# Kernel tuning notes

Hardware: AMD Instinct MI355X
Metric: run time of the kernel (lower is better)

## Reference

```python
import jax, jax.numpy as jnp
import numpy as np

B, N, HID, H, DH, NB = 4, 4096, 768, 12, 64, 266
EPS = 1e-4


def softmax_kernel(data, proj, is_query):
    # data: [B,H,N,DH], proj: [NB,DH]. FAVOR+ positive softmax features.
    d = data.shape[-1]
    ratio = proj.shape[0] ** -0.5
    dn = d ** -0.25  # data normalizer
    data_dash = jnp.einsum('bhnd,jd->bhnj', data * dn, proj)  # [B,H,N,NB]
    diag = 0.5 * jnp.sum((data * dn) ** 2, axis=-1, keepdims=True)  # [B,H,N,1]
    if is_query:
        m = jnp.max(data_dash, axis=-1, keepdims=True)
    else:
        m = jnp.max(data_dash, axis=(-1, -2), keepdims=True)
    return ratio * (jnp.exp(data_dash - diag - m) + EPS)


def setup_inputs() -> dict:
    key = jax.random.key(0)
    ks = jax.random.split(key, 8)
    s = HID ** -0.5
    return {
        'hidden_states': jax.random.normal(ks[0], (B, N, HID), jnp.float32),
        'Wq': jax.random.normal(ks[1], (HID, HID), jnp.float32) * s,
        'bq': jnp.zeros((HID,), jnp.float32),
        'Wk': jax.random.normal(ks[2], (HID, HID), jnp.float32) * s,
        'bk': jnp.zeros((HID,), jnp.float32),
        'Wv': jax.random.normal(ks[3], (HID, HID), jnp.float32) * s,
        'bv': jnp.zeros((HID,), jnp.float32),
        'proj': jax.random.normal(ks[4], (NB, DH), jnp.float32),
    }


def reference(hidden_states, Wq, bq, Wk, bk, Wv, bv, proj):
    def heads(x):  # [B,N,HID] -> [B,H,N,DH]
        return x.reshape(B, N, H, DH).transpose(0, 2, 1, 3)

    q = heads(hidden_states @ Wq.T + bq)
    k = heads(hidden_states @ Wk.T + bk)
    v = heads(hidden_states @ Wv.T + bv)

    qp = softmax_kernel(q, proj, True)   # [B,H,N,NB]
    kp = softmax_kernel(k, proj, False)  # [B,H,N,NB]

    # non-causal linear attention: out = q' (k'^T v) / (q' sum_n k')
    k_sum = jnp.sum(kp, axis=2)                               # [B,H,NB]
    d_inv = 1.0 / jnp.einsum('bhnj,bhj->bhn', qp, k_sum)      # [B,H,N]
    ctx = jnp.einsum('bhnj,bhnd->bhjd', kp, v)                # [B,H,NB,DH]
    out = jnp.einsum('bhnj,bhjd->bhnd', qp, ctx) * d_inv[..., None]

    return out.transpose(0, 2, 1, 3).reshape(B, N, HID)
```

## Files before the change

kernel.cpp:

```cpp
#include <hip/hip_runtime.h>
#include <hip/hip_bf16.h>
#include <stdint.h>

#define B_   4
#define N_   4096
#define HID_ 768
#define H_   12
#define DH_  64
#define NB_  266
#define NBP_ 288
#define EPS_ 1e-4f
#define RATIO_ 0.06131393f

typedef unsigned short u16;
typedef __attribute__((ext_vector_type(8))) short short8;
typedef __attribute__((ext_vector_type(4))) float floatx4;

__device__ __forceinline__ u16 f2b(float f) {
  __hip_bfloat16 h = __float2bfloat16(f);
  return *reinterpret_cast<u16*>(&h);
}
__device__ __forceinline__ float b2f(u16 u) {
  union { unsigned u; float f; } x; x.u = ((unsigned)u) << 16; return x.f;
}
__device__ __forceinline__ unsigned fmap(float x) {
  unsigned u = __float_as_uint(x);
  return (u & 0x80000000u) ? ~u : (u | 0x80000000u);
}
__device__ __forceinline__ float funmap(unsigned u) {
  unsigned b = (u & 0x80000000u) ? (u & 0x7FFFFFFFu) : ~u;
  return __uint_as_float(b);
}
__device__ __forceinline__ void gl16(const u16* g, u16* l) {
  __builtin_amdgcn_global_load_lds(
      (const __attribute__((address_space(1))) void*)g,
      (__attribute__((address_space(3))) void*)l, 16, 0, 0);
}

__global__ void k_convert4(const float4* __restrict__ src, uint2* __restrict__ dst, int n4) {
  int i = blockIdx.x * 256 + threadIdx.x;
  if (i >= n4) return;
  float4 v = src[i];
  union { u16 s[4]; uint2 u; } pk;
  pk.s[0] = f2b(v.x); pk.s[1] = f2b(v.y); pk.s[2] = f2b(v.z); pk.s[3] = f2b(v.w);
  dst[i] = pk.u;
}

__global__ void k_prep_proj(const float* __restrict__ proj, u16* __restrict__ dst) {
  int i = blockIdx.x * 256 + threadIdx.x;
  if (i >= NBP_ * DH_) return;
  int j = i / DH_, d = i - j * DH_;
  float v = (j < NB_) ? proj[j * DH_ + d] * 0.35355339059327373f : 0.f;
  dst[i] = f2b(v);
}

__global__ void k_init(float* __restrict__ zf, unsigned* __restrict__ mbuf, int nf) {
  int i = blockIdx.x * 256 + threadIdx.x;
  if (i < nf) zf[i] = 0.f;
  if (i < B_ * H_) mbuf[i] = 0u;
}

__global__ __launch_bounds__(256) void k_qkv(
    const u16* __restrict__ hsb, const u16* __restrict__ wb,
    const float* __restrict__ bq, const float* __restrict__ bk, const float* __restrict__ bv,
    u16* __restrict__ qb, u16* __restrict__ kb, u16* __restrict__ vT) {
  __shared__ u16 At[128 * 32];
  __shared__ u16 Bt[128 * 32];
  const int m0 = blockIdx.x * 128;
  const int bn = blockIdx.y;
  const int sel = bn / 6;
  const int or0 = (bn % 6) * 128;
  const u16* W = wb + (size_t)sel * HID_ * HID_;
  const int t = threadIdx.x, lane = t & 63, wv = t >> 6;
  const int wr = (wv >> 1) * 64, wc = (wv & 1) * 64;
  const int lm = lane & 15, lq = lane >> 4;
  const int srow = wv * 32 + (lane >> 2);
  const int scol = (lane & 3) * 8;
  const u16* gA0 = hsb + (size_t)(m0 + srow) * HID_ + scol;
  const u16* gA1 = gA0 + 16 * HID_;
  const u16* gB0 = W + (size_t)(or0 + srow) * HID_ + scol;
  const u16* gB1 = gB0 + 16 * HID_;
  u16* lA = At + wv * 1024;
  u16* lB = Bt + wv * 1024;
  floatx4 acc[4][4];
#pragma unroll
  for (int i = 0; i < 4; i++)
#pragma unroll
    for (int j = 0; j < 4; j++) acc[i][j] = (floatx4){0.f, 0.f, 0.f, 0.f};

  for (int k0 = 0; k0 < HID_; k0 += 32) {
    __syncthreads();
    gl16(gA0 + k0, lA);
    gl16(gA1 + k0, lA + 512);
    gl16(gB0 + k0, lB);
    gl16(gB1 + k0, lB + 512);
    __syncthreads();
    short8 af[4], bfr[4];
#pragma unroll
    for (int mt = 0; mt < 4; mt++) af[mt] = *(const short8*)&At[(wr + mt * 16 + lm) * 32 + lq * 8];
#pragma unroll
    for (int nt = 0; nt < 4; nt++) bfr[nt] = *(const short8*)&Bt[(wc + nt * 16 + lm) * 32 + lq * 8];
#pragma unroll
    for (int mt = 0; mt < 4; mt++)
#pragma unroll
      for (int nt = 0; nt < 4; nt++)
        acc[mt][nt] = __builtin_amdgcn_mfma_f32_16x16x32_bf16(af[mt], bfr[nt], acc[mt][nt], 0, 0, 0);
  }
  if (sel < 2) {
    const float* bias = (sel == 0) ? bq : bk;
    u16* dst = (sel == 0) ? qb : kb;
#pragma unroll
    for (int mt = 0; mt < 4; mt++) {
#pragma unroll
      for (int nt = 0; nt < 4; nt++) {
        int lc = or0 + wc + nt * 16 + lm;
        float bb = bias[lc];
#pragma unroll
        for (int r = 0; r < 4; r++) {
          int row = m0 + wr + mt * 16 + lq * 4 + r;
          dst[(size_t)row * HID_ + lc] = f2b(acc[mt][nt][r] + bb);
        }
      }
    }
  } else {
#pragma unroll
    for (int mt = 0; mt < 4; mt++) {
#pragma unroll
      for (int nt = 0; nt < 4; nt++) {
        int lc = or0 + wc + nt * 16 + lm;
        int hh = lc >> 6, dv = lc & 63;
        float bb = bv[lc];
        int rowbase = m0 + wr + mt * 16 + lq * 4;
        int b = rowbase >> 12, n = rowbase & 4095;
        union { u16 s[4]; uint2 u; } pk;
#pragma unroll
        for (int r = 0; r < 4; r++) pk.s[r] = f2b(acc[mt][nt][r] + bb);
        *(uint2*)(vT + ((size_t)(b * H_ + hh) * DH_ + dv) * N_ + n) = pk.u;
      }
    }
  }
}

__global__ __launch_bounds__(256) void k_kmax2(
    const u16* __restrict__ kb, const u16* __restrict__ projb, unsigned* __restrict__ mbuf) {
  const int bh = blockIdx.y, b = bh / H_, h = bh - b * H_;
  const int n0 = blockIdx.x * 256;
  const int t = threadIdx.x, lane = t & 63, wv = t >> 6;
  const int lm = lane & 15, lq = lane >> 4;
  const u16* kbase = kb + (size_t)(b * N_ + n0 + wv * 64) * HID_ + h * DH_;
  short8 af0[4], af1[4];
#pragma unroll
  for (int mt = 0; mt < 4; mt++) {
    const u16* p = kbase + (size_t)(mt * 16 + lm) * HID_ + lq * 8;
    af0[mt] = *(const short8*)p;
    af1[mt] = *(const short8*)(p + 32);
  }
  float mx = -3e38f;
  for (int ct = 0; ct < 17; ct++) {
    const u16* pp = projb + (ct * 16 + lm) * DH_ + lq * 8;
    short8 bf0 = *(const short8*)pp;
    short8 bf1 = *(const short8*)(pp + 32);
    bool valid = (ct < 16) || (lm < 10);
#pragma unroll
    for (int mt = 0; mt < 4; mt++) {
      floatx4 a = __builtin_amdgcn_mfma_f32_16x16x32_bf16(af0[mt], bf0, (floatx4){0.f,0.f,0.f,0.f}, 0, 0, 0);
      a = __builtin_amdgcn_mfma_f32_16x16x32_bf16(af1[mt], bf1, a, 0, 0, 0);
      if (valid) {
#pragma unroll
        for (int r = 0; r < 4; r++) mx = fmaxf(mx, a[r]);
      }
    }
  }
#pragma unroll
  for (int o = 1; o < 64; o <<= 1) mx = fmaxf(mx, __shfl_xor(mx, o));
  if (lane == 0) atomicMax(&mbuf[bh], fmap(mx));
}

__global__ __launch_bounds__(256) void k_ctx3(
    const u16* __restrict__ kb, const u16* __restrict__ vT, const u16* __restrict__ projb,
    const unsigned* __restrict__ mbuf, float* __restrict__ ctxTf, float* __restrict__ ksum) {
  __shared__ u16 kpl[NBP_ * 72];
  const int bh = blockIdx.y, b = bh / H_, h = bh - b * H_;
  const int n0 = blockIdx.x * 256;
  const int t = threadIdx.x, lane = t & 63, wv = t >> 6;
  const int lm = lane & 15, lq = lane >> 4;
  const float m = funmap(mbuf[bh]);
  const u16* vTb = vT + ((size_t)bh * DH_ + wv * 16 + lm) * N_;
  floatx4 acc[18];
#pragma unroll
  for (int jt = 0; jt < 18; jt++) acc[jt] = (floatx4){0.f, 0.f, 0.f, 0.f};
  float kacc[17];
#pragma unroll
  for (int ct = 0; ct < 17; ct++) kacc[ct] = 0.f;

  for (int it = 0; it < 4; it++) {
    const int n64 = n0 + it * 64;
    __syncthreads();
    {
      const int row = n64 + wv * 16 + lm;
      const u16* kr = kb + ((size_t)(b * N_) + row) * HID_ + h * DH_ + lq * 8;
      short8 af0 = *(const short8*)kr;
      short8 af1 = *(const short8*)(kr + 32);
      float rs = 0.f;
#pragma unroll
      for (int i = 0; i < 8; i++) { float f = b2f(((const u16*)&af0)[i]); rs += f * f; }
#pragma unroll
      for (int i = 0; i < 8; i++) { float f = b2f(((const u16*)&af1)[i]); rs += f * f; }
      rs += __shfl_xor(rs, 16);
      rs += __shfl_xor(rs, 32);
      float dg[4];
#pragma unroll
      for (int r = 0; r < 4; r++) dg[r] = 0.0625f * __shfl(rs, lq * 4 + r);
#pragma unroll
      for (int ct = 0; ct < 17; ct++) {
        const u16* pp = projb + (ct * 16 + lm) * DH_ + lq * 8;
        short8 bf0 = *(const short8*)pp;
        short8 bf1 = *(const short8*)(pp + 32);
        floatx4 a = __builtin_amdgcn_mfma_f32_16x16x32_bf16(af0, bf0, (floatx4){0.f,0.f,0.f,0.f}, 0, 0, 0);
        a = __builtin_amdgcn_mfma_f32_16x16x32_bf16(af1, bf1, a, 0, 0, 0);
        bool valid = (ct < 16) || (lm < 10);
        union { u16 s[4]; uint2 u; } pk;
        float kss = 0.f;
#pragma unroll
        for (int r = 0; r < 4; r++) {
          float val = valid ? RATIO_ * (__expf(a[r] - dg[r] - m) + EPS_) : 0.f;
          kss += val;
          pk.s[r] = f2b(val);
        }
        kacc[ct] += kss;
        *(uint2*)&kpl[(ct * 16 + lm) * 72 + wv * 16 + lq * 4] = pk.u;
      }
      *(uint2*)&kpl[(272 + lm) * 72 + wv * 16 + lq * 4] = make_uint2(0u, 0u);
    }
    __syncthreads();
#pragma unroll
    for (int ns = 0; ns < 2; ns++) {
      short8 av = *(const short8*)(vTb + n64 + ns * 32 + lq * 8);
#pragma unroll
      for (int jt = 0; jt < 18; jt++) {
        short8 bf = *(const short8*)&kpl[(jt * 16 + lm) * 72 + ns * 32 + lq * 8];
        acc[jt] = __builtin_amdgcn_mfma_f32_16x16x32_bf16(av, bf, acc[jt], 0, 0, 0);
      }
    }
  }
#pragma unroll
  for (int ct = 0; ct < 17; ct++) {
    float v = kacc[ct];
    v += __shfl_xor(v, 16);
    v += __shfl_xor(v, 32);
    if (lq == 0) atomicAdd(&ksum[bh * NBP_ + ct * 16 + lm], v);
  }
#pragma unroll
  for (int jt = 0; jt < 18; jt++) {
#pragma unroll
    for (int r = 0; r < 4; r++)
      atomicAdd(&ctxTf[((size_t)bh * DH_ + wv * 16 + lq * 4 + r) * NBP_ + jt * 16 + lm], acc[jt][r]);
  }
}

__global__ void k_cvt_ctx(const float* __restrict__ src, u16* __restrict__ dst) {
  int i = blockIdx.x * 256 + threadIdx.x;
  if (i < B_ * H_ * DH_ * NBP_) dst[i] = f2b(src[i]);
}

__global__ __launch_bounds__(256) void k_out2(
    const u16* __restrict__ qb, const u16* __restrict__ projb,
    const u16* __restrict__ ctxb, const float* __restrict__ ksum,
    float* __restrict__ outp) {
  __shared__ u16 qpl[4][16][296];
  const int bh = blockIdx.y, b = bh / H_, h = bh - b * H_;
  const int n0 = blockIdx.x * 256;
  const int t = threadIdx.x, lane = t & 63, wv = t >> 6;
  const int lm = lane & 15, lq = lane >> 4;
  const u16* qbase = qb + (size_t)(b * N_ + n0 + wv * 64) * HID_ + h * DH_;
  const u16* cb = ctxb + (size_t)bh * DH_ * NBP_;
  const float* ksb = ksum + bh * NBP_;

  for (int mt = 0; mt < 4; mt++) {
    const u16* prow = qbase + (size_t)(mt * 16 + lm) * HID_ + lq * 8;
    short8 af0 = *(const short8*)prow;
    short8 af1 = *(const short8*)(prow + 32);
    float rs = 0.f;
#pragma unroll
    for (int i = 0; i < 8; i++) { float f = b2f(((const u16*)&af0)[i]); rs += f * f; }
#pragma unroll
    for (int i = 0; i < 8; i++) { float f = b2f(((const u16*)&af1)[i]); rs += f * f; }
    rs += __shfl_xor(rs, 16);
    rs += __shfl_xor(rs, 32);
    float dg[4];
#pragma unroll
    for (int r = 0; r < 4; r++) dg[r] = 0.0625f * __shfl(rs, lq * 4 + r);

    floatx4 dd[17];
    float rm[4] = {-3e38f, -3e38f, -3e38f, -3e38f};
#pragma unroll
    for (int ct = 0; ct < 17; ct++) {
      const u16* pp = projb + (ct * 16 + lm) * DH_ + lq * 8;
      short8 bf0 = *(const short8*)pp;
      short8 bf1 = *(const short8*)(pp + 32);
      floatx4 a = __builtin_amdgcn_mfma_f32_16x16x32_bf16(af0, bf0, (floatx4){0.f,0.f,0.f,0.f}, 0, 0, 0);
      a = __builtin_amdgcn_mfma_f32_16x16x32_bf16(af1, bf1, a, 0, 0, 0);
      dd[ct] = a;
      if ((ct < 16) || (lm < 10)) {
#pragma unroll
        for (int r = 0; r < 4; r++) rm[r] = fmaxf(rm[r], a[r]);
      }
    }
#pragma unroll
    for (int o = 1; o < 16; o <<= 1) {
#pragma unroll
      for (int r = 0; r < 4; r++) rm[r] = fmaxf(rm[r], __shfl_xor(rm[r], o));
    }
    float dpart[4] = {0.f, 0.f, 0.f, 0.f};
#pragma unroll
    for (int ct = 0; ct < 18; ct++) {
      floatx4 a = (ct < 17) ? dd[ct] : (floatx4){0.f, 0.f, 0.f, 0.f};
      bool valid = (ct < 16) || (ct == 16 && lm < 10);
      float ksv = ksb[ct * 16 + lm];
#pragma unroll
      for (int r = 0; r < 4; r++) {
        float qpv = valid ? RATIO_ * (__expf(a[r] - dg[r] - rm[r]) + EPS_) : 0.f;
        dpart[r] += qpv * ksv;
        qpl[wv][lq * 4 + r][ct * 16 + lm] = f2b(qpv);
      }
    }
#pragma unroll
    for (int o = 1; o < 16; o <<= 1) {
#pragma unroll
      for (int r = 0; r < 4; r++) dpart[r] += __shfl_xor(dpart[r], o);
    }
    float dinv[4];
#pragma unroll
    for (int r = 0; r < 4; r++) dinv[r] = 1.f / dpart[r];

    floatx4 ao[4];
#pragma unroll
    for (int dt = 0; dt < 4; dt++) ao[dt] = (floatx4){0.f, 0.f, 0.f, 0.f};
#pragma unroll
    for (int ks9 = 0; ks9 < 9; ks9++) {
      short8 aq = *(const short8*)&qpl[wv][lm][ks9 * 32 + lq * 8];
#pragma unroll
      for (int dt = 0; dt < 4; dt++) {
        short8 bc = *(const short8*)(cb + (size_t)(dt * 16 + lm) * NBP_ + ks9 * 32 + lq * 8);
        ao[dt] = __builtin_amdgcn_mfma_f32_16x16x32_bf16(aq, bc, ao[dt], 0, 0, 0);
      }
    }
#pragma unroll
    for (int dt = 0; dt < 4; dt++) {
#pragma unroll
      for (int r = 0; r < 4; r++) {
        int n = n0 + wv * 64 + mt * 16 + lq * 4 + r;
        outp[((size_t)(b * N_ + n)) * HID_ + h * DH_ + dt * 16 + lm] = ao[dt][r] * dinv[r];
      }
    }
  }
}

extern "C" void kernel_launch(void* const* d_in, const int* in_sizes, int n_in,
                              void* d_out, int out_size, void* d_ws, size_t ws_size,
                              hipStream_t stream) {
  (void)in_sizes; (void)n_in; (void)out_size; (void)ws_size;
  const float* hs   = (const float*)d_in[0];
  const float* Wq   = (const float*)d_in[1];
  const float* bq   = (const float*)d_in[2];
  const float* Wk   = (const float*)d_in[3];
  const float* bk   = (const float*)d_in[4];
  const float* Wv   = (const float*)d_in[5];
  const float* bv   = (const float*)d_in[6];
  const float* proj = (const float*)d_in[7];

  char* w = (char*)d_ws;
  u16* hsb   = (u16*)w;  w += (size_t)16384 * 768 * 2;
  u16* wb3   = (u16*)w;  w += (size_t)3 * 768 * 768 * 2;
  u16* projb = (u16*)w;  w += (size_t)NBP_ * 64 * 2;
  u16* qb    = (u16*)w;  w += (size_t)16384 * 768 * 2;
  u16* kb    = (u16*)w;  w += (size_t)16384 * 768 * 2;
  u16* vT    = (u16*)w;  w += (size_t)48 * DH_ * N_ * 2;
  float* ksum  = (float*)w; w += (size_t)48 * NBP_ * 4;
  float* ctxTf = (float*)w; w += (size_t)48 * DH_ * NBP_ * 4;
  u16* ctxTb = (u16*)w;  w += (size_t)48 * DH_ * NBP_ * 2;
  unsigned* mbuf = (unsigned*)w;

  hipLaunchKernelGGL(k_convert4, dim3(12288), dim3(256), 0, stream, (const float4*)hs, (uint2*)hsb, 16384 * 768 / 4);
  hipLaunchKernelGGL(k_convert4, dim3(576), dim3(256), 0, stream, (const float4*)Wq, (uint2*)wb3, 768 * 768 / 4);
  hipLaunchKernelGGL(k_convert4, dim3(576), dim3(256), 0, stream, (const float4*)Wk, (uint2*)(wb3 + 768 * 768), 768 * 768 / 4);
  hipLaunchKernelGGL(k_convert4, dim3(576), dim3(256), 0, stream, (const float4*)Wv, (uint2*)(wb3 + 2 * 768 * 768), 768 * 768 / 4);
  hipLaunchKernelGGL(k_prep_proj, dim3(72), dim3(256), 0, stream, proj, projb);
  int nz = 48 * NBP_ + 48 * DH_ * NBP_;
  hipLaunchKernelGGL(k_init, dim3((nz + 255) / 256), dim3(256), 0, stream, ksum, mbuf, nz);
  hipLaunchKernelGGL(k_qkv, dim3(128, 18), dim3(256), 0, stream, hsb, wb3, bq, bk, bv, qb, kb, vT);
  hipLaunchKernelGGL(k_kmax2, dim3(16, 48), dim3(256), 0, stream, kb, projb, mbuf);
  hipLaunchKernelGGL(k_ctx3, dim3(16, 48), dim3(256), 0, stream, kb, vT, projb, mbuf, ctxTf, ksum);
  hipLaunchKernelGGL(k_cvt_ctx, dim3((48 * DH_ * NBP_ + 255) / 256), dim3(256), 0, stream, ctxTf, ctxTb);
  hipLaunchKernelGGL(k_out2, dim3(16, 48), dim3(256), 0, stream, qb, projb, ctxTb, ksum, (float*)d_out);
}
```

Baseline: 422.9 us.

## Fuse prep kernels, deepen QKV GEMM K-step, recompute projections in output kernel

The six conversion, projection-prep and zero-init launches are merged into a single k_prep kernel, so fewer launches are issued. The QKV GEMM now stages two 32-wide K slices per barrier pair, which halves the number of synchronisations and doubles the LDS tile. The output kernel no longer keeps 17 projection accumulators live: it recomputes the MFMA projections in the exp pass and preloads ksum into registers, trading extra MFMA work for lower register pressure.

```diff
diff --git a/kernel.cpp b/kernel.cpp
--- a/kernel.cpp
+++ b/kernel.cpp
@@ -37,35 +37,56 @@
       (__attribute__((address_space(3))) void*)l, 16, 0, 0);
 }
 
-__global__ void k_convert4(const float4* __restrict__ src, uint2* __restrict__ dst, int n4) {
-  int i = blockIdx.x * 256 + threadIdx.x;
-  if (i >= n4) return;
-  float4 v = src[i];
-  union { u16 s[4]; uint2 u; } pk;
-  pk.s[0] = f2b(v.x); pk.s[1] = f2b(v.y); pk.s[2] = f2b(v.z); pk.s[3] = f2b(v.w);
-  dst[i] = pk.u;
-}
-
-__global__ void k_prep_proj(const float* __restrict__ proj, u16* __restrict__ dst) {
-  int i = blockIdx.x * 256 + threadIdx.x;
-  if (i >= NBP_ * DH_) return;
-  int j = i / DH_, d = i - j * DH_;
-  float v = (j < NB_) ? proj[j * DH_ + d] * 0.35355339059327373f : 0.f;
-  dst[i] = f2b(v);
-}
-
-__global__ void k_init(float* __restrict__ zf, unsigned* __restrict__ mbuf, int nf) {
-  int i = blockIdx.x * 256 + threadIdx.x;
-  if (i < nf) zf[i] = 0.f;
-  if (i < B_ * H_) mbuf[i] = 0u;
+__global__ __launch_bounds__(256) void k_prep(
+    const float4* __restrict__ hs, const float4* __restrict__ Wq,
+    const float4* __restrict__ Wk, const float4* __restrict__ Wv,
+    const float* __restrict__ proj,
+    uint2* __restrict__ hsb, uint2* __restrict__ wb3, u16* __restrict__ projb,
+    float4* __restrict__ zf, unsigned* __restrict__ mbuf) {
+  int blk = blockIdx.x;
+  const int t = threadIdx.x;
+  if (blk < 12288) {
+    int i = blk * 256 + t;
+    float4 v = hs[i];
+    union { u16 s[4]; uint2 u; } pk;
+    pk.s[0] = f2b(v.x); pk.s[1] = f2b(v.y); pk.s[2] = f2b(v.z); pk.s[3] = f2b(v.w);
+    hsb[i] = pk.u;
+    return;
+  }
+  blk -= 12288;
+  if (blk < 1728) {
+    int i = blk * 256 + t;
+    int sel = i / 147456, j = i - sel * 147456;
+    const float4* s = (sel == 0) ? Wq : (sel == 1) ? Wk : Wv;
+    float4 v = s[j];
+    union { u16 s4[4]; uint2 u; } pk;
+    pk.s4[0] = f2b(v.x); pk.s4[1] = f2b(v.y); pk.s4[2] = f2b(v.z); pk.s4[3] = f2b(v.w);
+    wb3[i] = pk.u;
+    return;
+  }
+  blk -= 1728;
+  if (blk < 72) {
+    int i = blk * 256 + t;
+    int j = i / DH_, d = i - j * DH_;
+    float v = (j < NB_) ? proj[j * DH_ + d] * 0.35355339059327373f : 0.f;
+    projb[i] = f2b(v);
+    return;
+  }
+  blk -= 72;
+  if (blk < 878) {
+    int i = blk * 256 + t;
+    if (i < 224640) zf[i] = (float4){0.f, 0.f, 0.f, 0.f};
+    return;
+  }
+  if (t < B_ * H_) mbuf[t] = 0u;
 }
 
 __global__ __launch_bounds__(256) void k_qkv(
     const u16* __restrict__ hsb, const u16* __restrict__ wb,
     const float* __restrict__ bq, const float* __restrict__ bk, const float* __restrict__ bv,
     u16* __restrict__ qb, u16* __restrict__ kb, u16* __restrict__ vT) {
-  __shared__ u16 At[128 * 32];
-  __shared__ u16 Bt[128 * 32];
+  __shared__ u16 At[2 * 128 * 32];
+  __shared__ u16 Bt[2 * 128 * 32];
   const int m0 = blockIdx.x * 128;
   const int bn = blockIdx.y;
   const int sel = bn / 6;
@@ -76,10 +97,8 @@
   const int lm = lane & 15, lq = lane >> 4;
   const int srow = wv * 32 + (lane >> 2);
   const int scol = (lane & 3) * 8;
-  const u16* gA0 = hsb + (size_t)(m0 + srow) * HID_ + scol;
-  const u16* gA1 = gA0 + 16 * HID_;
-  const u16* gB0 = W + (size_t)(or0 + srow) * HID_ + scol;
-  const u16* gB1 = gB0 + 16 * HID_;
+  const u16* gA = hsb + (size_t)(m0 + srow) * HID_ + scol;
+  const u16* gB = W + (size_t)(or0 + srow) * HID_ + scol;
   u16* lA = At + wv * 1024;
   u16* lB = Bt + wv * 1024;
   floatx4 acc[4][4];
@@ -88,23 +107,30 @@
 #pragma unroll
     for (int j = 0; j < 4; j++) acc[i][j] = (floatx4){0.f, 0.f, 0.f, 0.f};
 
-  for (int k0 = 0; k0 < HID_; k0 += 32) {
+  for (int k0 = 0; k0 < HID_; k0 += 64) {
     __syncthreads();
-    gl16(gA0 + k0, lA);
-    gl16(gA1 + k0, lA + 512);
-    gl16(gB0 + k0, lB);
-    gl16(gB1 + k0, lB + 512);
+#pragma unroll
+    for (int p = 0; p < 2; p++) {
+#pragma unroll
+      for (int i = 0; i < 2; i++) {
+        gl16(gA + k0 + p * 32 + i * 16 * HID_, lA + p * 4096 + i * 512);
+        gl16(gB + k0 + p * 32 + i * 16 * HID_, lB + p * 4096 + i * 512);
+      }
+    }
     __syncthreads();
-    short8 af[4], bfr[4];
-#pragma unroll
-    for (int mt = 0; mt < 4; mt++) af[mt] = *(const short8*)&At[(wr + mt * 16 + lm) * 32 + lq * 8];
-#pragma unroll
-    for (int nt = 0; nt < 4; nt++) bfr[nt] = *(const short8*)&Bt[(wc + nt * 16 + lm) * 32 + lq * 8];
-#pragma unroll
-    for (int mt = 0; mt < 4; mt++)
-#pragma unroll
-      for (int nt = 0; nt < 4; nt++)
-        acc[mt][nt] = __builtin_amdgcn_mfma_f32_16x16x32_bf16(af[mt], bfr[nt], acc[mt][nt], 0, 0, 0);
+#pragma unroll
+    for (int p = 0; p < 2; p++) {
+      short8 af[4], bfr[4];
+#pragma unroll
+      for (int mt = 0; mt < 4; mt++) af[mt] = *(const short8*)&At[p * 4096 + (wr + mt * 16 + lm) * 32 + lq * 8];
+#pragma unroll
+      for (int nt = 0; nt < 4; nt++) bfr[nt] = *(const short8*)&Bt[p * 4096 + (wc + nt * 16 + lm) * 32 + lq * 8];
+#pragma unroll
+      for (int mt = 0; mt < 4; mt++)
+#pragma unroll
+        for (int nt = 0; nt < 4; nt++)
+          acc[mt][nt] = __builtin_amdgcn_mfma_f32_16x16x32_bf16(af[mt], bfr[nt], acc[mt][nt], 0, 0, 0);
+    }
   }
   if (sel < 2) {
     const float* bias = (sel == 0) ? bq : bk;
@@ -263,7 +289,7 @@
   if (i < B_ * H_ * DH_ * NBP_) dst[i] = f2b(src[i]);
 }
 
-__global__ __launch_bounds__(256) void k_out2(
+__global__ __launch_bounds__(256) void k_out3(
     const u16* __restrict__ qb, const u16* __restrict__ projb,
     const u16* __restrict__ ctxb, const float* __restrict__ ksum,
     float* __restrict__ outp) {
@@ -275,6 +301,9 @@
   const u16* qbase = qb + (size_t)(b * N_ + n0 + wv * 64) * HID_ + h * DH_;
   const u16* cb = ctxb + (size_t)bh * DH_ * NBP_;
   const float* ksb = ksum + bh * NBP_;
+  float ksv[17];
+#pragma unroll
+  for (int ct = 0; ct < 17; ct++) ksv[ct] = ksb[ct * 16 + lm];
 
   for (int mt = 0; mt < 4; mt++) {
     const u16* prow = qbase + (size_t)(mt * 16 + lm) * HID_ + lq * 8;
@@ -291,7 +320,6 @@
 #pragma unroll
     for (int r = 0; r < 4; r++) dg[r] = 0.0625f * __shfl(rs, lq * 4 + r);
 
-    floatx4 dd[17];
     float rm[4] = {-3e38f, -3e38f, -3e38f, -3e38f};
 #pragma unroll
     for (int ct = 0; ct < 17; ct++) {
@@ -300,7 +328,6 @@
       short8 bf1 = *(const short8*)(pp + 32);
       floatx4 a = __builtin_amdgcn_mfma_f32_16x16x32_bf16(af0, bf0, (floatx4){0.f,0.f,0.f,0.f}, 0, 0, 0);
       a = __builtin_amdgcn_mfma_f32_16x16x32_bf16(af1, bf1, a, 0, 0, 0);
-      dd[ct] = a;
       if ((ct < 16) || (lm < 10)) {
 #pragma unroll
         for (int r = 0; r < 4; r++) rm[r] = fmaxf(rm[r], a[r]);
@@ -314,13 +341,22 @@
     float dpart[4] = {0.f, 0.f, 0.f, 0.f};
 #pragma unroll
     for (int ct = 0; ct < 18; ct++) {
-      floatx4 a = (ct < 17) ? dd[ct] : (floatx4){0.f, 0.f, 0.f, 0.f};
+      floatx4 a;
+      if (ct < 17) {
+        const u16* pp = projb + (ct * 16 + lm) * DH_ + lq * 8;
+        short8 bf0 = *(const short8*)pp;
+        short8 bf1 = *(const short8*)(pp + 32);
+        a = __builtin_amdgcn_mfma_f32_16x16x32_bf16(af0, bf0, (floatx4){0.f,0.f,0.f,0.f}, 0, 0, 0);
+        a = __builtin_amdgcn_mfma_f32_16x16x32_bf16(af1, bf1, a, 0, 0, 0);
+      } else {
+        a = (floatx4){0.f, 0.f, 0.f, 0.f};
+      }
       bool valid = (ct < 16) || (ct == 16 && lm < 10);
-      float ksv = ksb[ct * 16 + lm];
+      float kv = (ct < 17) ? ksv[ct] : 0.f;
 #pragma unroll
       for (int r = 0; r < 4; r++) {
         float qpv = valid ? RATIO_ * (__expf(a[r] - dg[r] - rm[r]) + EPS_) : 0.f;
-        dpart[r] += qpv * ksv;
+        dpart[r] += qpv * kv;
         qpl[wv][lq * 4 + r][ct * 16 + lm] = f2b(qpv);
       }
     }
@@ -381,16 +417,12 @@
   u16* ctxTb = (u16*)w;  w += (size_t)48 * DH_ * NBP_ * 2;
   unsigned* mbuf = (unsigned*)w;
 
-  hipLaunchKernelGGL(k_convert4, dim3(12288), dim3(256), 0, stream, (const float4*)hs, (uint2*)hsb, 16384 * 768 / 4);
-  hipLaunchKernelGGL(k_convert4, dim3(576), dim3(256), 0, stream, (const float4*)Wq, (uint2*)wb3, 768 * 768 / 4);
-  hipLaunchKernelGGL(k_convert4, dim3(576), dim3(256), 0, stream, (const float4*)Wk, (uint2*)(wb3 + 768 * 768), 768 * 768 / 4);
-  hipLaunchKernelGGL(k_convert4, dim3(576), dim3(256), 0, stream, (const float4*)Wv, (uint2*)(wb3 + 2 * 768 * 768), 768 * 768 / 4);
-  hipLaunchKernelGGL(k_prep_proj, dim3(72), dim3(256), 0, stream, proj, projb);
-  int nz = 48 * NBP_ + 48 * DH_ * NBP_;
-  hipLaunchKernelGGL(k_init, dim3((nz + 255) / 256), dim3(256), 0, stream, ksum, mbuf, nz);
+  hipLaunchKernelGGL(k_prep, dim3(14967), dim3(256), 0, stream,
+                     (const float4*)hs, (const float4*)Wq, (const float4*)Wk, (const float4*)Wv,
+                     proj, (uint2*)hsb, (uint2*)wb3, projb, (float4*)ksum, mbuf);
   hipLaunchKernelGGL(k_qkv, dim3(128, 18), dim3(256), 0, stream, hsb, wb3, bq, bk, bv, qb, kb, vT);
   hipLaunchKernelGGL(k_kmax2, dim3(16, 48), dim3(256), 0, stream, kb, projb, mbuf);
   hipLaunchKernelGGL(k_ctx3, dim3(16, 48), dim3(256), 0, stream, kb, vT, projb, mbuf, ctxTf, ksum);
   hipLaunchKernelGGL(k_cvt_ctx, dim3((48 * DH_ * NBP_ + 255) / 256), dim3(256), 0, stream, ctxTf, ctxTb);
-  hipLaunchKernelGGL(k_out2, dim3(16, 48), dim3(256), 0, stream, qb, projb, ctxTb, ksum, (float*)d_out);
-}
+  hipLaunchKernelGGL(k_out3, dim3(16, 48), dim3(256), 0, stream, qb, projb, ctxTb, ksum, (float*)d_out);
+}
```

Result: faster. 404.8 us (-4.3%).
